# Kernel optimization log

Hardware: AMD Instinct MI355X
Metric: run time of the kernel (lower is better)

## Reference

```python
import jax, jax.numpy as jnp
import numpy as np

B, S, D, H = 4, 2048, 768, 12
HD = D // H  # 64


def setup_inputs() -> dict:
    key = jax.random.key(0)
    ks = jax.random.split(key, 6)
    sc = 0.02
    return {
        "x": jax.random.normal(ks[0], (B, S, D), dtype=jnp.float32),
        "wq": jax.random.normal(ks[1], (D, D), dtype=jnp.float32) * sc,
        "wk": jax.random.normal(ks[2], (D, D), dtype=jnp.float32) * sc,
        "wv": jax.random.normal(ks[3], (D, D), dtype=jnp.float32) * sc,
        "wo": jax.random.normal(ks[4], (D, D), dtype=jnp.float32) * sc,
        "bo": jnp.zeros((D,), dtype=jnp.float32),
    }


def reference(x, wq, wk, wv, wo, bo):
    b, s, d = x.shape
    # nn.Linear applies x @ W^T; project then split heads -> [b, h, s, hd]
    def heads(w):
        return (x @ w.T).reshape(b, s, H, HD).transpose(0, 2, 1, 3)
    q, k, v = heads(wq), heads(wk), heads(wv)
    scores = jnp.einsum("bhqd,bhkd->bhqk", q, k)
    causal = jnp.triu(jnp.ones((s, s), dtype=bool), 1)
    # original masks with -inf BEFORE scaling; -inf/sqrt(d) == -inf, same softmax
    scores = jnp.where(causal, -jnp.inf, scores) / jnp.sqrt(jnp.float32(HD))
    attn = jax.nn.softmax(scores, axis=-1)  # dropout=0.0 (eval/deterministic)
    ctx = jnp.einsum("bhqk,bhkd->bhqd", attn, v)
    ctx = ctx.transpose(0, 2, 1, 3).reshape(b, s, d)
    return ctx @ wo.T + bo
```

## Files before the change

### kernel.cpp

```cpp
#include <hip/hip_runtime.h>

#define B_ 4
#define S_ 2048
#define D_ 768
#define H_ 12
#define HD_ 64
#define T_ (B_ * S_)

typedef __bf16 bf16x8 __attribute__((ext_vector_type(8)));
typedef __bf16 bf16x4 __attribute__((ext_vector_type(4)));
typedef float  f32x4  __attribute__((ext_vector_type(4)));

__device__ __forceinline__ f32x4 mfma16(bf16x8 a, bf16x8 b, f32x4 c) {
  return __builtin_amdgcn_mfma_f32_16x16x32_bf16(a, b, c, 0, 0, 0);
}

__device__ __forceinline__ float fexp2(float x) {
  float r;
  asm("v_exp_f32 %0, %1" : "=v"(r) : "v"(x));
  return r;
}

__device__ __forceinline__ void gload16(const __bf16* g, __bf16* lds) {
  __builtin_amdgcn_global_load_lds(
      (__attribute__((address_space(1))) void*)g,
      (__attribute__((address_space(3))) void*)lds, 16, 0, 0);
}

__global__ void cvt_all(const float* __restrict__ x,
                        const float* __restrict__ wq,
                        const float* __restrict__ wk,
                        const float* __restrict__ wv,
                        const float* __restrict__ wo,
                        __bf16* __restrict__ out) {
  constexpr int XN4 = T_ * D_ / 4;
  constexpr int WN4 = D_ * D_ / 4;
  const int i = blockIdx.x * blockDim.x + threadIdx.x;
  if (i >= XN4 + 4 * WN4) return;
  const float* src;
  int k;
  float scale = 1.0f;
  if (i < XN4) {
    src = x;
    k = i;
  } else {
    const int j = i - XN4;
    const int wsel = j / WN4;
    k = j - wsel * WN4;
    src = (wsel == 0) ? wq : (wsel == 1) ? wk : (wsel == 2) ? wv : wo;
    if (wsel == 1) scale = 0.18033688f;
  }
  const float4 v = reinterpret_cast<const float4*>(src)[k];
  bf16x4 o;
  o[0] = (__bf16)(v.x * scale);
  o[1] = (__bf16)(v.y * scale);
  o[2] = (__bf16)(v.z * scale);
  o[3] = (__bf16)(v.w * scale);
  reinterpret_cast<bf16x4*>(out)[i] = o;
}

template <int MODE>
__global__ __launch_bounds__(256)
__attribute__((amdgpu_waves_per_eu(2)))
void gemm_bt(const __bf16* __restrict__ A,
             const __bf16* __restrict__ W0, const __bf16* __restrict__ W1,
             const __bf16* __restrict__ W2,
             __bf16* __restrict__ Oq, __bf16* __restrict__ Ok,
             __bf16* __restrict__ Ov,
             float* __restrict__ fout, const float* __restrict__ bias) {
  constexpr int K = D_;
  constexpr int NT = K / 64;
  __shared__ __align__(16) __bf16 sA[2][128 * 64];
  __shared__ __align__(16) __bf16 sB[2][128 * 64];

  const int tid = threadIdx.x;
  const int l = tid & 63;
  const int w = tid >> 6;

  const int flat = blockIdx.y * 64 + blockIdx.x;
  const int xcd = flat & 7;
  const int q = flat >> 3;
  const int mtile = xcd * 8 + (q & 7);
  const int pan = q >> 3;
  const int m0 = mtile * 128;

  int mat, n0;
  const __bf16* Wm;
  if (MODE == 0) {
    mat = pan / 6;
    n0 = (pan % 6) * 128;
    Wm = (mat == 0) ? W0 : (mat == 1) ? W1 : W2;
  } else {
    mat = 0;
    n0 = pan * 128;
    Wm = W0;
  }

  const int srow = l >> 3;
  const int scol = ((l & 7) ^ srow) * 8;
  const __bf16* gA[4];
  const __bf16* gB[4];
#pragma unroll
  for (int i = 0; i < 4; ++i) {
    const int c = w * 4 + i;
    gA[i] = A + (size_t)(m0 + c * 8 + srow) * K + scol;
    gB[i] = Wm + (size_t)(n0 + c * 8 + srow) * K + scol;
  }

  f32x4 acc[4][4] = {};
  const int wr = w >> 1, wc = w & 1;
  const int fr = l & 15, fq = l >> 4;
  const int swz = (fr & 7) << 4;

#pragma unroll
  for (int i = 0; i < 4; ++i) {
    const int c = w * 4 + i;
    gload16(gA[i], &sA[0][c * 512]);
    gload16(gB[i], &sB[0][c * 512]);
  }
#pragma unroll
  for (int i = 0; i < 4; ++i) {
    const int c = w * 4 + i;
    gload16(gA[i] + 64, &sA[1][c * 512]);
    gload16(gB[i] + 64, &sB[1][c * 512]);
  }

  int cur = 0;
  for (int kt = 0; kt < NT; ++kt) {
    if (kt + 1 < NT)
      asm volatile("s_waitcnt vmcnt(8)" ::: "memory");
    else
      asm volatile("s_waitcnt vmcnt(0)" ::: "memory");
    __builtin_amdgcn_s_barrier();

    const char* ab = reinterpret_cast<const char*>(&sA[cur][0]);
    const char* bb = reinterpret_cast<const char*>(&sB[cur][0]);
#pragma unroll
    for (int ks = 0; ks < 2; ++ks) {
      bf16x8 af[4], bfr[4];
#pragma unroll
      for (int mi = 0; mi < 4; ++mi)
        af[mi] = *reinterpret_cast<const bf16x8*>(
            ab + (wr * 64 + mi * 16 + fr) * 128 +
            ((ks * 64 + fq * 16) ^ swz));
#pragma unroll
      for (int ni = 0; ni < 4; ++ni)
        bfr[ni] = *reinterpret_cast<const bf16x8*>(
            bb + (wc * 64 + ni * 16 + fr) * 128 +
            ((ks * 64 + fq * 16) ^ swz));
#pragma unroll
      for (int mi = 0; mi < 4; ++mi)
#pragma unroll
        for (int ni = 0; ni < 4; ++ni)
          acc[mi][ni] = mfma16(af[mi], bfr[ni], acc[mi][ni]);
    }
    __builtin_amdgcn_s_barrier();

    if (kt + 2 < NT) {
      const int ko = (kt + 2) * 64;
#pragma unroll
      for (int i = 0; i < 4; ++i) {
        const int c = w * 4 + i;
        gload16(gA[i] + ko, &sA[cur][c * 512]);
        gload16(gB[i] + ko, &sB[cur][c * 512]);
      }
    }
    cur ^= 1;
  }

#pragma unroll
  for (int mi = 0; mi < 4; ++mi) {
    const int mbase = m0 + wr * 64 + mi * 16 + fq * 4;
#pragma unroll
    for (int ni = 0; ni < 4; ++ni) {
      const int o = n0 + wc * 64 + ni * 16 + fr;
      if (MODE == 1) {
#pragma unroll
        for (int r = 0; r < 4; ++r)
          fout[(mbase + r) * D_ + o] = acc[mi][ni][r] + bias[o];
      } else {
        const int h = o >> 6, hd = o & 63;
        const int b = mbase >> 11, s = mbase & (S_ - 1);
        if (mat == 2) {
          bf16x4 vv;
#pragma unroll
          for (int r = 0; r < 4; ++r) vv[r] = (__bf16)acc[mi][ni][r];
          *reinterpret_cast<bf16x4*>(
              &Ov[((size_t)((b * H_ + h) * HD_ + hd)) * S_ + s]) = vv;
        } else {
          __bf16* dst = (mat == 0) ? Oq : Ok;
#pragma unroll
          for (int r = 0; r < 4; ++r)
            dst[((size_t)((b * H_ + h) * S_ + s + r)) * HD_ + hd] =
                (__bf16)acc[mi][ni][r];
        }
      }
    }
  }
}

__global__ __launch_bounds__(256)
__attribute__((amdgpu_waves_per_eu(3, 4)))
void attn_kernel(const __bf16* __restrict__ Q, const __bf16* __restrict__ Kt,
                 const __bf16* __restrict__ Vt, __bf16* __restrict__ C) {
  __shared__ __align__(16) __bf16 sK[2][64 * 64];
  __shared__ __align__(16) __bf16 sV[2][64 * 64];
  __shared__ __align__(16) __bf16 sP[4][32 * 64];

  const int tid = threadIdx.x;
  const int l = tid & 63;
  const int w = tid >> 6;
  const int fr = l & 15, fq = l >> 4;
  const int bx = blockIdx.x;
  const int xcd = bx & 7;
  const int j = bx >> 3;
  const int bh = xcd + 8 * (j % 6);
  const int qtile = 15 - j / 6;
  const int qb = qtile * 128;
  const int qbw = qb + w * 32;

  const __bf16* qh = Q + (size_t)bh * S_ * HD_;
  const __bf16* kh = Kt + (size_t)bh * S_ * HD_;
  const __bf16* vh = Vt + (size_t)bh * HD_ * S_;
  char* sPb = reinterpret_cast<char*>(&sP[w][0]);

  const int srow = l >> 3;
  const int scol = ((l & 7) * 8) ^ (srow << 3);
  const int swz = (fr & 7) << 4;

  bf16x8 qf[2][2];
#pragma unroll
  for (int g = 0; g < 2; ++g)
#pragma unroll
    for (int ks = 0; ks < 2; ++ks)
      qf[g][ks] = *reinterpret_cast<const bf16x8*>(
          &qh[(size_t)(qbw + g * 16 + fr) * HD_ + ks * 32 + fq * 8]);

  f32x4 acc[2][4] = {};
  float mrow[2] = {-1e30f, -1e30f}, lrow[2] = {0.f, 0.f};

  const int nt = qb / 64 + 2;
  int cur = 0;

  {
    const int q0 = 2 * w, q1 = 2 * w + 1;
    gload16(kh + (size_t)(q0 * 8 + srow) * HD_ + scol, &sK[0][q0 * 512]);
    gload16(kh + (size_t)(q1 * 8 + srow) * HD_ + scol, &sK[0][q1 * 512]);
    gload16(vh + (size_t)(q0 * 8 + srow) * S_ + scol, &sV[0][q0 * 512]);
    gload16(vh + (size_t)(q1 * 8 + srow) * S_ + scol, &sV[0][q1 * 512]);
  }
  __syncthreads();

  for (int t = 0; t < nt; ++t) {
    const int kv0 = t * 64;
    if (t + 1 < nt) {
      const int kvn = kv0 + 64;
      const int q0 = 2 * w, q1 = 2 * w + 1;
      gload16(kh + (size_t)(kvn + q0 * 8 + srow) * HD_ + scol,
              &sK[cur ^ 1][q0 * 512]);
      gload16(kh + (size_t)(kvn + q1 * 8 + srow) * HD_ + scol,
              &sK[cur ^ 1][q1 * 512]);
      gload16(vh + (size_t)(q0 * 8 + srow) * S_ + kvn + scol,
              &sV[cur ^ 1][q0 * 512]);
      gload16(vh + (size_t)(q1 * 8 + srow) * S_ + kvn + scol,
              &sV[cur ^ 1][q1 * 512]);
    }

    if (kv0 <= qbw + 31) {
      const char* kb = reinterpret_cast<const char*>(&sK[cur][0]);
      const char* vb = reinterpret_cast<const char*>(&sV[cur][0]);

      f32x4 s[2][4];
      __builtin_amdgcn_s_setprio(1);
#pragma unroll
      for (int c = 0; c < 4; ++c) {
        const int row = c * 16 + fr;
        bf16x8 kf0 = *reinterpret_cast<const bf16x8*>(
            kb + row * 128 + ((fq * 16) ^ swz));
        bf16x8 kf1 = *reinterpret_cast<const bf16x8*>(
            kb + row * 128 + ((fq * 16 + 64) ^ swz));
#pragma unroll
        for (int g = 0; g < 2; ++g) {
          f32x4 z = {};
          z = mfma16(kf0, qf[g][0], z);
          z = mfma16(kf1, qf[g][1], z);
          s[g][c] = z;
        }
      }
      __builtin_amdgcn_s_setprio(0);

      if (kv0 + 63 > qbw) {
#pragma unroll
        for (int g = 0; g < 2; ++g) {
          const int qi = qbw + g * 16 + fr;
#pragma unroll
          for (int c = 0; c < 4; ++c)
#pragma unroll
            for (int r = 0; r < 4; ++r) {
              const int kvi = kv0 + c * 16 + fq * 4 + r;
              if (kvi > qi) s[g][c][r] = -1e30f;
            }
        }
      }

#pragma unroll
      for (int g = 0; g < 2; ++g) {
        float tm = -1e30f;
#pragma unroll
        for (int c = 0; c < 4; ++c)
#pragma unroll
          for (int r = 0; r < 4; ++r) tm = fmaxf(tm, s[g][c][r]);
        tm = fmaxf(tm, __shfl_xor(tm, 16));
        tm = fmaxf(tm, __shfl_xor(tm, 32));
        const float mn = fmaxf(mrow[g], tm);
        const float fac = fexp2(mrow[g] - mn);
        mrow[g] = mn;
        float sum = 0.f;
#pragma unroll
        for (int c = 0; c < 4; ++c) {
          bf16x4 pc;
#pragma unroll
          for (int r = 0; r < 4; ++r) {
            const float p = fexp2(s[g][c][r] - mn);
            sum += p;
            pc[r] = (__bf16)p;
          }
          const int bo = (c * 32 + fq * 8) ^ swz;
          *reinterpret_cast<bf16x4*>(sPb + (g * 16 + fr) * 128 + bo) = pc;
        }
        sum += __shfl_xor(sum, 16);
        sum += __shfl_xor(sum, 32);
        lrow[g] = lrow[g] * fac + sum;
#pragma unroll
        for (int dt = 0; dt < 4; ++dt)
#pragma unroll
          for (int r = 0; r < 4; ++r) acc[g][dt][r] *= fac;

        bf16x8 pa[2];
#pragma unroll
        for (int ks = 0; ks < 2; ++ks) {
          const int bo = (ks * 64 + fq * 16) ^ swz;
          pa[ks] = *reinterpret_cast<const bf16x8*>(sPb +
                                                    (g * 16 + fr) * 128 + bo);
        }

        __builtin_amdgcn_s_setprio(1);
#pragma unroll
        for (int dt = 0; dt < 4; ++dt) {
          const int row = dt * 16 + fr;
          bf16x8 vf0 = *reinterpret_cast<const bf16x8*>(
              vb + row * 128 + ((fq * 16) ^ swz));
          bf16x8 vf1 = *reinterpret_cast<const bf16x8*>(
              vb + row * 128 + ((fq * 16 + 64) ^ swz));
          acc[g][dt] = mfma16(vf0, pa[0], acc[g][dt]);
          acc[g][dt] = mfma16(vf1, pa[1], acc[g][dt]);
        }
        __builtin_amdgcn_s_setprio(0);
      }
    }

    __syncthreads();
    cur ^= 1;
  }

  const int b = bh / H_, h = bh % H_;
#pragma unroll
  for (int g = 0; g < 2; ++g) {
    const float inv_l = 1.0f / lrow[g];
    const int qrow = qbw + g * 16 + fr;
#pragma unroll
    for (int dt = 0; dt < 4; ++dt) {
      bf16x4 ov;
#pragma unroll
      for (int r = 0; r < 4; ++r) ov[r] = (__bf16)(acc[g][dt][r] * inv_l);
      *reinterpret_cast<bf16x4*>(
          &C[((size_t)(b * S_ + qrow)) * D_ + h * HD_ + dt * 16 + fq * 4]) =
          ov;
    }
  }
}

static constexpr size_t XB_OFF = 0;
static constexpr size_t WQ_OFF = XB_OFF + (size_t)T_ * D_;
static constexpr size_t WK_OFF = WQ_OFF + (size_t)D_ * D_;
static constexpr size_t WV_OFF = WK_OFF + (size_t)D_ * D_;
static constexpr size_t WO_OFF = WV_OFF + (size_t)D_ * D_;
static constexpr size_t Q_OFF = WO_OFF + (size_t)D_ * D_;
static constexpr size_t K_OFF = Q_OFF + (size_t)T_ * D_;
static constexpr size_t V_OFF = K_OFF + (size_t)T_ * D_;
static constexpr size_t C_OFF = V_OFF + (size_t)T_ * D_;

extern "C" void kernel_launch(void* const* d_in, const int* in_sizes, int n_in,
                              void* d_out, int out_size, void* d_ws,
                              size_t ws_size, hipStream_t stream) {
  const float* x = (const float*)d_in[0];
  const float* wq = (const float*)d_in[1];
  const float* wk = (const float*)d_in[2];
  const float* wv = (const float*)d_in[3];
  const float* wo = (const float*)d_in[4];
  const float* bo = (const float*)d_in[5];
  float* out = (float*)d_out;
  __bf16* ws = (__bf16*)d_ws;

  __bf16* xb = ws + XB_OFF;
  __bf16* wqb = ws + WQ_OFF;
  __bf16* wkb = ws + WK_OFF;
  __bf16* wvb = ws + WV_OFF;
  __bf16* wob = ws + WO_OFF;
  __bf16* qbuf = ws + Q_OFF;
  __bf16* kbuf = ws + K_OFF;
  __bf16* vbuf = ws + V_OFF;
  __bf16* cbuf = ws + C_OFF;

  {
    constexpr int n4 = T_ * D_ / 4 + 4 * (D_ * D_ / 4);
    cvt_all<<<(n4 + 255) / 256, 256, 0, stream>>>(x, wq, wk, wv, wo, ws);
  }

  gemm_bt<0><<<dim3(64, 18), 256, 0, stream>>>(
      xb, wqb, wkb, wvb, qbuf, kbuf, vbuf, nullptr, nullptr);

  attn_kernel<<<dim3(768), 256, 0, stream>>>(qbuf, kbuf, vbuf, cbuf);

  gemm_bt<1><<<dim3(64, 6), 256, 0, stream>>>(
      cbuf, wob, nullptr, nullptr, nullptr, nullptr, nullptr, out, bo);
}
```

Before: 128.5 us.

## Prefetch two KV tiles ahead, defer softmax rescale, rebalance causal block order

Measured after the change: 130.7 us. Within noise of the previous version (+1.7%).

```diff
diff --git a/kernel.cpp b/kernel.cpp
--- a/kernel.cpp
+++ b/kernel.cpp
@@ -214,8 +214,15 @@
   const int bx = blockIdx.x;
   const int xcd = bx & 7;
   const int j = bx >> 3;
-  const int bh = xcd + 8 * (j % 6);
-  const int qtile = 15 - j / 6;
+  const int L = j >> 5;
+  const int u = j & 31;
+  const int i = u & 15;
+  const int rep = u >> 4;
+  int qtile;
+  if (L == 0) qtile = 15 - i;
+  else if (L == 1) qtile = (i < 8) ? 2 * i : 2 * i - 15;
+  else qtile = (i < 8) ? 7 - i : 23 - i;
+  const int bh = xcd + 8 * (2 * L + rep);
   const int qb = qtile * 128;
   const int qbw = qb + w * 32;
 
@@ -241,31 +248,25 @@
 
   const int nt = qb / 64 + 2;
   int cur = 0;
-
-  {
-    const int q0 = 2 * w, q1 = 2 * w + 1;
-    gload16(kh + (size_t)(q0 * 8 + srow) * HD_ + scol, &sK[0][q0 * 512]);
-    gload16(kh + (size_t)(q1 * 8 + srow) * HD_ + scol, &sK[0][q1 * 512]);
-    gload16(vh + (size_t)(q0 * 8 + srow) * S_ + scol, &sV[0][q0 * 512]);
-    gload16(vh + (size_t)(q1 * 8 + srow) * S_ + scol, &sV[0][q1 * 512]);
-  }
-  __syncthreads();
+  const int q0 = 2 * w, q1 = 2 * w + 1;
+
+  gload16(kh + (size_t)(q0 * 8 + srow) * HD_ + scol, &sK[0][q0 * 512]);
+  gload16(kh + (size_t)(q1 * 8 + srow) * HD_ + scol, &sK[0][q1 * 512]);
+  gload16(vh + (size_t)(q0 * 8 + srow) * S_ + scol, &sV[0][q0 * 512]);
+  gload16(vh + (size_t)(q1 * 8 + srow) * S_ + scol, &sV[0][q1 * 512]);
+  gload16(kh + (size_t)(64 + q0 * 8 + srow) * HD_ + scol, &sK[1][q0 * 512]);
+  gload16(kh + (size_t)(64 + q1 * 8 + srow) * HD_ + scol, &sK[1][q1 * 512]);
+  gload16(vh + (size_t)(q0 * 8 + srow) * S_ + 64 + scol, &sV[1][q0 * 512]);
+  gload16(vh + (size_t)(q1 * 8 + srow) * S_ + 64 + scol, &sV[1][q1 * 512]);
 
   for (int t = 0; t < nt; ++t) {
+    if (t + 1 < nt)
+      asm volatile("s_waitcnt vmcnt(4)" ::: "memory");
+    else
+      asm volatile("s_waitcnt vmcnt(0)" ::: "memory");
+    __builtin_amdgcn_s_barrier();
+
     const int kv0 = t * 64;
-    if (t + 1 < nt) {
-      const int kvn = kv0 + 64;
-      const int q0 = 2 * w, q1 = 2 * w + 1;
-      gload16(kh + (size_t)(kvn + q0 * 8 + srow) * HD_ + scol,
-              &sK[cur ^ 1][q0 * 512]);
-      gload16(kh + (size_t)(kvn + q1 * 8 + srow) * HD_ + scol,
-              &sK[cur ^ 1][q1 * 512]);
-      gload16(vh + (size_t)(q0 * 8 + srow) * S_ + kvn + scol,
-              &sV[cur ^ 1][q0 * 512]);
-      gload16(vh + (size_t)(q1 * 8 + srow) * S_ + kvn + scol,
-              &sV[cur ^ 1][q1 * 512]);
-    }
-
     if (kv0 <= qbw + 31) {
       const char* kb = reinterpret_cast<const char*>(&sK[cur][0]);
       const char* vb = reinterpret_cast<const char*>(&sV[cur][0]);
@@ -312,9 +313,17 @@
           for (int r = 0; r < 4; ++r) tm = fmaxf(tm, s[g][c][r]);
         tm = fmaxf(tm, __shfl_xor(tm, 16));
         tm = fmaxf(tm, __shfl_xor(tm, 32));
-        const float mn = fmaxf(mrow[g], tm);
-        const float fac = fexp2(mrow[g] - mn);
-        mrow[g] = mn;
+        const bool defer = __all(tm - mrow[g] <= 8.0f);
+        const float mn = defer ? mrow[g] : fmaxf(mrow[g], tm);
+        if (!defer) {
+          const float fac = fexp2(mrow[g] - mn);
+          mrow[g] = mn;
+          lrow[g] *= fac;
+#pragma unroll
+          for (int dt = 0; dt < 4; ++dt)
+#pragma unroll
+            for (int r = 0; r < 4; ++r) acc[g][dt][r] *= fac;
+        }
         float sum = 0.f;
 #pragma unroll
         for (int c = 0; c < 4; ++c) {
@@ -330,11 +339,7 @@
         }
         sum += __shfl_xor(sum, 16);
         sum += __shfl_xor(sum, 32);
-        lrow[g] = lrow[g] * fac + sum;
-#pragma unroll
-        for (int dt = 0; dt < 4; ++dt)
-#pragma unroll
-          for (int r = 0; r < 4; ++r) acc[g][dt][r] *= fac;
+        lrow[g] += sum;
 
         bf16x8 pa[2];
 #pragma unroll
@@ -359,7 +364,19 @@
       }
     }
 
-    __syncthreads();
+    __builtin_amdgcn_s_barrier();
+
+    if (t + 2 < nt) {
+      const int kvn = (t + 2) * 64;
+      gload16(kh + (size_t)(kvn + q0 * 8 + srow) * HD_ + scol,
+              &sK[cur][q0 * 512]);
+      gload16(kh + (size_t)(kvn + q1 * 8 + srow) * HD_ + scol,
+              &sK[cur][q1 * 512]);
+      gload16(vh + (size_t)(q0 * 8 + srow) * S_ + kvn + scol,
+              &sV[cur][q0 * 512]);
+      gload16(vh + (size_t)(q1 * 8 + srow) * S_ + kvn + scol,
+              &sV[cur][q1 * 512]);
+    }
     cur ^= 1;
   }
 
```

## Halve attention query tile to 64 rows and double grid size

Applied to the files above, without the earlier changes.

After: 121.3 us. 1.06x faster.

```diff
diff --git a/kernel.cpp b/kernel.cpp
--- a/kernel.cpp
+++ b/kernel.cpp
@@ -200,12 +200,12 @@
 }
 
 __global__ __launch_bounds__(256)
-__attribute__((amdgpu_waves_per_eu(3, 4)))
+__attribute__((amdgpu_waves_per_eu(4, 4)))
 void attn_kernel(const __bf16* __restrict__ Q, const __bf16* __restrict__ Kt,
                  const __bf16* __restrict__ Vt, __bf16* __restrict__ C) {
   __shared__ __align__(16) __bf16 sK[2][64 * 64];
   __shared__ __align__(16) __bf16 sV[2][64 * 64];
-  __shared__ __align__(16) __bf16 sP[4][32 * 64];
+  __shared__ __align__(16) __bf16 sP[4][16 * 64];
 
   const int tid = threadIdx.x;
   const int l = tid & 63;
@@ -215,9 +215,9 @@
   const int xcd = bx & 7;
   const int j = bx >> 3;
   const int bh = xcd + 8 * (j % 6);
-  const int qtile = 15 - j / 6;
-  const int qb = qtile * 128;
-  const int qbw = qb + w * 32;
+  const int qtile = 31 - j / 6;
+  const int qb = qtile * 64;
+  const int qbw = qb + w * 16;
 
   const __bf16* qh = Q + (size_t)bh * S_ * HD_;
   const __bf16* kh = Kt + (size_t)bh * S_ * HD_;
@@ -228,34 +228,29 @@
   const int scol = ((l & 7) * 8) ^ (srow << 3);
   const int swz = (fr & 7) << 4;
 
-  bf16x8 qf[2][2];
-#pragma unroll
-  for (int g = 0; g < 2; ++g)
-#pragma unroll
-    for (int ks = 0; ks < 2; ++ks)
-      qf[g][ks] = *reinterpret_cast<const bf16x8*>(
-          &qh[(size_t)(qbw + g * 16 + fr) * HD_ + ks * 32 + fq * 8]);
-
-  f32x4 acc[2][4] = {};
-  float mrow[2] = {-1e30f, -1e30f}, lrow[2] = {0.f, 0.f};
-
-  const int nt = qb / 64 + 2;
+  bf16x8 qf[2];
+#pragma unroll
+  for (int ks = 0; ks < 2; ++ks)
+    qf[ks] = *reinterpret_cast<const bf16x8*>(
+        &qh[(size_t)(qbw + fr) * HD_ + ks * 32 + fq * 8]);
+
+  f32x4 acc[4] = {};
+  float mrow = -1e30f, lrow = 0.f;
+
+  const int nt = qtile + 1;
   int cur = 0;
-
-  {
-    const int q0 = 2 * w, q1 = 2 * w + 1;
-    gload16(kh + (size_t)(q0 * 8 + srow) * HD_ + scol, &sK[0][q0 * 512]);
-    gload16(kh + (size_t)(q1 * 8 + srow) * HD_ + scol, &sK[0][q1 * 512]);
-    gload16(vh + (size_t)(q0 * 8 + srow) * S_ + scol, &sV[0][q0 * 512]);
-    gload16(vh + (size_t)(q1 * 8 + srow) * S_ + scol, &sV[0][q1 * 512]);
-  }
+  const int q0 = 2 * w, q1 = 2 * w + 1;
+
+  gload16(kh + (size_t)(q0 * 8 + srow) * HD_ + scol, &sK[0][q0 * 512]);
+  gload16(kh + (size_t)(q1 * 8 + srow) * HD_ + scol, &sK[0][q1 * 512]);
+  gload16(vh + (size_t)(q0 * 8 + srow) * S_ + scol, &sV[0][q0 * 512]);
+  gload16(vh + (size_t)(q1 * 8 + srow) * S_ + scol, &sV[0][q1 * 512]);
   __syncthreads();
 
   for (int t = 0; t < nt; ++t) {
     const int kv0 = t * 64;
     if (t + 1 < nt) {
       const int kvn = kv0 + 64;
-      const int q0 = 2 * w, q1 = 2 * w + 1;
       gload16(kh + (size_t)(kvn + q0 * 8 + srow) * HD_ + scol,
               &sK[cur ^ 1][q0 * 512]);
       gload16(kh + (size_t)(kvn + q1 * 8 + srow) * HD_ + scol,
@@ -266,11 +261,11 @@
               &sV[cur ^ 1][q1 * 512]);
     }
 
-    if (kv0 <= qbw + 31) {
+    if (kv0 <= qbw + 15) {
       const char* kb = reinterpret_cast<const char*>(&sK[cur][0]);
       const char* vb = reinterpret_cast<const char*>(&sV[cur][0]);
 
-      f32x4 s[2][4];
+      f32x4 s[4];
       __builtin_amdgcn_s_setprio(1);
 #pragma unroll
       for (int c = 0; c < 4; ++c) {
@@ -279,84 +274,74 @@
             kb + row * 128 + ((fq * 16) ^ swz));
         bf16x8 kf1 = *reinterpret_cast<const bf16x8*>(
             kb + row * 128 + ((fq * 16 + 64) ^ swz));
-#pragma unroll
-        for (int g = 0; g < 2; ++g) {
-          f32x4 z = {};
-          z = mfma16(kf0, qf[g][0], z);
-          z = mfma16(kf1, qf[g][1], z);
-          s[g][c] = z;
+        f32x4 z = {};
+        z = mfma16(kf0, qf[0], z);
+        z = mfma16(kf1, qf[1], z);
+        s[c] = z;
+      }
+      __builtin_amdgcn_s_setprio(0);
+
+      if (kv0 + 63 > qbw) {
+        const int qi = qbw + fr;
+#pragma unroll
+        for (int c = 0; c < 4; ++c)
+#pragma unroll
+          for (int r = 0; r < 4; ++r) {
+            const int kvi = kv0 + c * 16 + fq * 4 + r;
+            if (kvi > qi) s[c][r] = -1e30f;
+          }
+      }
+
+      float tm = -1e30f;
+#pragma unroll
+      for (int c = 0; c < 4; ++c)
+#pragma unroll
+        for (int r = 0; r < 4; ++r) tm = fmaxf(tm, s[c][r]);
+      tm = fmaxf(tm, __shfl_xor(tm, 16));
+      tm = fmaxf(tm, __shfl_xor(tm, 32));
+      const float mn = fmaxf(mrow, tm);
+      const float fac = fexp2(mrow - mn);
+      mrow = mn;
+      float sum = 0.f;
+#pragma unroll
+      for (int c = 0; c < 4; ++c) {
+        bf16x4 pc;
+#pragma unroll
+        for (int r = 0; r < 4; ++r) {
+          const float p = fexp2(s[c][r] - mn);
+          sum += p;
+          pc[r] = (__bf16)p;
         }
+        const int bo = (c * 32 + fq * 8) ^ swz;
+        *reinterpret_cast<bf16x4*>(sPb + fr * 128 + bo) = pc;
+      }
+      sum += __shfl_xor(sum, 16);
+      sum += __shfl_xor(sum, 32);
+      lrow = lrow * fac + sum;
+#pragma unroll
+      for (int dt = 0; dt < 4; ++dt)
+#pragma unroll
+        for (int r = 0; r < 4; ++r) acc[dt][r] *= fac;
+
+      bf16x8 pa[2];
+#pragma unroll
+      for (int ks = 0; ks < 2; ++ks) {
+        const int bo = (ks * 64 + fq * 16) ^ swz;
+        pa[ks] = *reinterpret_cast<const bf16x8*>(sPb + fr * 128 + bo);
+      }
+
+      __builtin_amdgcn_s_setprio(1);
+#pragma unroll
+      for (int dt = 0; dt < 4; ++dt) {
+        const int row = dt * 16 + fr;
+        bf16x8 vf0 = *reinterpret_cast<const bf16x8*>(
+            vb + row * 128 + ((fq * 16) ^ swz));
+        bf16x8 vf1 = *reinterpret_cast<const bf16x8*>(
+            vb + row * 128 + ((fq * 16 + 64) ^ swz));
+        acc[dt] = mfma16(vf0, pa[0], acc[dt]);
+        acc[dt] = mfma16(vf1, pa[1], acc[dt]);
       }
       __builtin_amdgcn_s_setprio(0);
-
-      if (kv0 + 63 > qbw) {
-#pragma unroll
-        for (int g = 0; g < 2; ++g) {
-          const int qi = qbw + g * 16 + fr;
-#pragma unroll
-          for (int c = 0; c < 4; ++c)
-#pragma unroll
-            for (int r = 0; r < 4; ++r) {
-              const int kvi = kv0 + c * 16 + fq * 4 + r;
-              if (kvi > qi) s[g][c][r] = -1e30f;
-            }
-        }
-      }
-
-#pragma unroll
-      for (int g = 0; g < 2; ++g) {
-        float tm = -1e30f;
-#pragma unroll
-        for (int c = 0; c < 4; ++c)
-#pragma unroll
-          for (int r = 0; r < 4; ++r) tm = fmaxf(tm, s[g][c][r]);
-        tm = fmaxf(tm, __shfl_xor(tm, 16));
-        tm = fmaxf(tm, __shfl_xor(tm, 32));
-        const float mn = fmaxf(mrow[g], tm);
-        const float fac = fexp2(mrow[g] - mn);
-        mrow[g] = mn;
-        float sum = 0.f;
-#pragma unroll
-        for (int c = 0; c < 4; ++c) {
-          bf16x4 pc;
-#pragma unroll
-          for (int r = 0; r < 4; ++r) {
-            const float p = fexp2(s[g][c][r] - mn);
-            sum += p;
-            pc[r] = (__bf16)p;
-          }
-          const int bo = (c * 32 + fq * 8) ^ swz;
-          *reinterpret_cast<bf16x4*>(sPb + (g * 16 + fr) * 128 + bo) = pc;
-        }
-        sum += __shfl_xor(sum, 16);
-        sum += __shfl_xor(sum, 32);
-        lrow[g] = lrow[g] * fac + sum;
-#pragma unroll
-        for (int dt = 0; dt < 4; ++dt)
-#pragma unroll
-          for (int r = 0; r < 4; ++r) acc[g][dt][r] *= fac;
-
-        bf16x8 pa[2];
-#pragma unroll
-        for (int ks = 0; ks < 2; ++ks) {
-          const int bo = (ks * 64 + fq * 16) ^ swz;
-          pa[ks] = *reinterpret_cast<const bf16x8*>(sPb +
-                                                    (g * 16 + fr) * 128 + bo);
-        }
-
-        __builtin_amdgcn_s_setprio(1);
-#pragma unroll
-        for (int dt = 0; dt < 4; ++dt) {
-          const int row = dt * 16 + fr;
-          bf16x8 vf0 = *reinterpret_cast<const bf16x8*>(
-              vb + row * 128 + ((fq * 16) ^ swz));
-          bf16x8 vf1 = *reinterpret_cast<const bf16x8*>(
-              vb + row * 128 + ((fq * 16 + 64) ^ swz));
-          acc[g][dt] = mfma16(vf0, pa[0], acc[g][dt]);
-          acc[g][dt] = mfma16(vf1, pa[1], acc[g][dt]);
-        }
-        __builtin_amdgcn_s_setprio(0);
-      }
     }
 
     __syncthreads();
@@ -364,19 +349,15 @@
   }
 
   const int b = bh / H_, h = bh % H_;
-#pragma unroll
-  for (int g = 0; g < 2; ++g) {
-    const float inv_l = 1.0f / lrow[g];
-    const int qrow = qbw + g * 16 + fr;
-#pragma unroll
-    for (int dt = 0; dt < 4; ++dt) {
-      bf16x4 ov;
-#pragma unroll
-      for (int r = 0; r < 4; ++r) ov[r] = (__bf16)(acc[g][dt][r] * inv_l);
-      *reinterpret_cast<bf16x4*>(
-          &C[((size_t)(b * S_ + qrow)) * D_ + h * HD_ + dt * 16 + fq * 4]) =
-          ov;
-    }
+  const float inv_l = 1.0f / lrow;
+  const int qrow = qbw + fr;
+#pragma unroll
+  for (int dt = 0; dt < 4; ++dt) {
+    bf16x4 ov;
+#pragma unroll
+    for (int r = 0; r < 4; ++r) ov[r] = (__bf16)(acc[dt][r] * inv_l);
+    *reinterpret_cast<bf16x4*>(
+        &C[((size_t)(b * S_ + qrow)) * D_ + h * HD_ + dt * 16 + fq * 4]) = ov;
   }
 }
 
@@ -420,7 +401,7 @@
   gemm_bt<0><<<dim3(64, 18), 256, 0, stream>>>(
       xb, wqb, wkb, wvb, qbuf, kbuf, vbuf, nullptr, nullptr);
 
-  attn_kernel<<<dim3(768), 256, 0, stream>>>(qbuf, kbuf, vbuf, cbuf);
+  attn_kernel<<<dim3(1536), 256, 0, stream>>>(qbuf, kbuf, vbuf, cbuf);
 
   gemm_bt<1><<<dim3(64, 6), 256, 0, stream>>>(
       cbuf, wob, nullptr, nullptr, nullptr, nullptr, nullptr, out, bo);
```
